# Performance work log

Measured on AMD Instinct MI355X. Metric: run time of the kernel, lower is better.

## Reference

```python
import jax, jax.numpy as jnp
import numpy as np

K = 3  # kernel_size
P = 1  # padding


def setup_inputs() -> dict:
    key = jax.random.key(0)
    k1, k2, k3 = jax.random.split(key, 3)
    B, Cin, H, W = 4, 64, 64, 64
    Cout = 64
    L = K * K + 1  # patch length + constant-1 term = 10
    x = jax.random.normal(k1, (B, Cin, H, W), dtype=jnp.float32)
    # kaiming_uniform-like scale for filters / biases
    filters = jax.random.normal(k2, (Cout, Cin, L, L), dtype=jnp.float32) * 0.05
    biases = jax.random.normal(k3, (Cout, 1), dtype=jnp.float32) * 0.05
    return {"x": x, "filters": filters, "biases": biases}


def reference(x, filters, biases):
    # x: [B, Cin, H, W]; filters: [Cout, Cin, L, L]; biases: [Cout, 1]
    B, C, H, W = x.shape
    xp = jnp.pad(x, ((0, 0), (0, 0), (P, P), (P, P)))
    # im2col: flattened KxK patch per pixel, row-major over (dy, dx) -> [B, C, K*K, H, W]
    patches = jnp.stack(
        [xp[:, :, dy:dy + H, dx:dx + W] for dy in range(K) for dx in range(K)],
        axis=2,
    )
    # prepend constant 1 -> s: [B, C, L, H, W], L = K*K + 1
    ones = jnp.ones((B, C, 1, H, W), dtype=x.dtype)
    s = jnp.concatenate([ones, patches], axis=2)
    # per-pixel, per-channel outer product s s^T: [B, C, L, L, H, W]
    outer = s[:, :, :, None, :, :] * s[:, :, None, :, :, :]
    # quadratic-form contraction with filters, summed over (c, i, j)
    out = jnp.einsum('bcijhw,ocij->bohw', outer, filters)
    out = out + biases[:, 0][None, :, None, None]
    return out
```

## Files before the change

kernel.cpp:

```cpp
#include <hip/hip_runtime.h>
#include <hip/hip_bf16.h>


typedef __attribute__((ext_vector_type(8))) short short8;
typedef __attribute__((ext_vector_type(16))) float f32x16;

#define NCH  64
#define NOUT 64

__device__ constexpr signed char TI[56] = {
  0,0,0,0,0,0,0,0,0,
  1,2,3,4,5,6,7,8,9,
  1,1,1,1,1,1,1,1,
  2,2,2,2,2,2,2,
  3,3,3,3,3,3,
  4,4,4,4,4,
  5,5,5,5,
  6,6,6,
  7,7,
  8,
  0,0};
__device__ constexpr signed char TJ[56] = {
  1,2,3,4,5,6,7,8,9,
  1,2,3,4,5,6,7,8,9,
  2,3,4,5,6,7,8,9,
  3,4,5,6,7,8,9,
  4,5,6,7,8,9,
  5,6,7,8,9,
  6,7,8,9,
  7,8,9,
  8,9,
  9,
  0,0};

__device__ __forceinline__ unsigned short f2bf(float f) {
  __hip_bfloat16 h = __float2bfloat16(f);
  unsigned short u;
  __builtin_memcpy(&u, &h, 2);
  return u;
}

__global__ __launch_bounds__(256) void prep_w2(const float* __restrict__ F,
                                               const float* __restrict__ biases,
                                               unsigned short* __restrict__ W2) {
  int idx = blockIdx.x * 256 + threadIdx.x;
  int e = idx & 7, o = (idx >> 3) & 63;
  int rest = idx >> 9;
  int hf = rest & 1, stp = rest >> 1;
  int st = stp % 7, pair = stp / 7;
  int ch = (st < 4) ? (2 * pair + hf) : (2 * pair + 1 - hf);
  int kl = (st < 4) ? (16 * st + e) : (16 * (st - 4) + 8 + e);
  const float* base = F + (size_t)(o * NCH + ch) * 100;
  float w;
  if (kl < 54) {
    int i = TI[kl], j = TJ[kl];
    if (i == 0)      w = base[j] + base[j * 10];
    else if (i == j) w = base[i * 10 + j];
    else             w = base[i * 10 + j] + base[j * 10 + i];
  } else if (kl == 54) {
    w = base[0] + (ch == 0 ? biases[o] : 0.f);
  } else {
    w = 0.f;
  }
  W2[idx] = f2bf(w);
}

__global__ __launch_bounds__(512, 2) void poly2d_mfma(
    const float* __restrict__ x, const unsigned short* __restrict__ W2,
    float* __restrict__ out) {
  const int b = blockIdx.x >> 6, h = blockIdx.x & 63;
  const int tid = threadIdx.x;
  const int lane = tid & 63, wave = tid >> 6;
  const int px = lane & 31, hf = lane >> 5;

  __shared__ float xs[NCH][3][66];
  __shared__ float R[8][64][32];

  #pragma unroll
  for (int it = 0; it < 25; ++it) {
    int idx = tid + it * 512;
    if (idx < NCH * 198) {
      int c = idx / 198, rem = idx % 198;
      int r = rem / 66, col = rem % 66;
      int hh = h + r - 1, ww = col - 1;
      float v = 0.f;
      if ((unsigned)hh < 64u && (unsigned)ww < 64u)
        v = x[(((size_t)b * NCH + c) * 64 + hh) * 64 + ww];
      xs[c][r][col] = v;
    }
  }
  __syncthreads();

  f32x16 a00, a01, a10, a11;
  #pragma unroll
  for (int r = 0; r < 16; ++r) { a00[r] = 0.f; a01[r] = 0.f; a10[r] = 0.f; a11[r] = 0.f; }

  auto computeP = [&](int cAl, int cBl, int pcol, short8* P) {
    float sA[9], sB[9];
    #pragma unroll
    for (int jm = 0; jm < 9; ++jm) {
      sA[jm] = xs[cAl][jm / 3][pcol + jm % 3];
      sB[jm] = xs[cBl][jm / 3][pcol + jm % 3];
    }
    #pragma unroll
    for (int g = 0; g < 7; ++g) {
      short8 pk;
      #pragma unroll
      for (int e = 0; e < 8; ++e) {
        const int kl = (g < 4) ? (16 * g + e) : (16 * (g - 4) + 8 + e);
        const float* s = (g < 4) ? sA : sB;
        float v;
        if (kl == 55)      v = 0.f;
        else if (kl == 54) v = 1.f;
        else if (kl < 9)   v = s[kl];
        else if (kl < 18)  { float t = s[kl - 9]; v = t * t; }
        else               v = s[TI[kl] - 1] * s[TJ[kl] - 1];
        pk[e] = (short)f2bf(v);
      }
      P[g] = pk;
    }
  };

  for (int stage = 0; stage < 4; ++stage) {
    const int cA = wave * 8 + stage * 2 + hf;
    const int cB = cA ^ 1;
    short8 P0[7], P1[7];
    computeP(cA, cB, px, P0);
    computeP(cA, cB, px + 32, P1);
    const unsigned short* wb =
        W2 + (size_t)(wave * 4 + stage) * 7168 + hf * 512 + px * 8;
    #pragma unroll
    for (int st = 0; st < 7; ++st) {
      const short8 w0 = *(const short8*)(wb + st * 1024);
      const short8 w1 = *(const short8*)(wb + st * 1024 + 256);
      a00 = __builtin_amdgcn_mfma_f32_32x32x16_bf16(w0, P0[st], a00, 0, 0, 0);
      a10 = __builtin_amdgcn_mfma_f32_32x32x16_bf16(w1, P0[st], a10, 0, 0, 0);
      a01 = __builtin_amdgcn_mfma_f32_32x32x16_bf16(w0, P1[st], a01, 0, 0, 0);
      a11 = __builtin_amdgcn_mfma_f32_32x32x16_bf16(w1, P1[st], a11, 0, 0, 0);
    }
  }

  #pragma unroll
  for (int r = 0; r < 16; ++r) {
    int orow = (r & 3) + 8 * (r >> 2) + 4 * hf;
    R[wave][orow][px]      = a00[r];
    R[wave][orow + 32][px] = a10[r];
  }
  __syncthreads();
  {
    int o = tid >> 3, p4 = (tid & 7) * 4;
    float4 sum = make_float4(0.f, 0.f, 0.f, 0.f);
    #pragma unroll
    for (int g = 0; g < 8; ++g) {
      float4 v = *(float4*)&R[g][o][p4];
      sum.x += v.x; sum.y += v.y; sum.z += v.z; sum.w += v.w;
    }
    *(float4*)&out[(((size_t)b * NOUT + o) * 64 + h) * 64 + p4] = sum;
  }
  __syncthreads();
  #pragma unroll
  for (int r = 0; r < 16; ++r) {
    int orow = (r & 3) + 8 * (r >> 2) + 4 * hf;
    R[wave][orow][px]      = a01[r];
    R[wave][orow + 32][px] = a11[r];
  }
  __syncthreads();
  {
    int o = tid >> 3, p4 = (tid & 7) * 4;
    float4 sum = make_float4(0.f, 0.f, 0.f, 0.f);
    #pragma unroll
    for (int g = 0; g < 8; ++g) {
      float4 v = *(float4*)&R[g][o][p4];
      sum.x += v.x; sum.y += v.y; sum.z += v.z; sum.w += v.w;
    }
    *(float4*)&out[(((size_t)b * NOUT + o) * 64 + h) * 64 + 32 + p4] = sum;
  }
}

extern "C" void kernel_launch(void* const* d_in, const int* in_sizes, int n_in,
                              void* d_out, int out_size, void* d_ws, size_t ws_size,
                              hipStream_t stream) {
  const float* x       = (const float*)d_in[0];
  const float* filters = (const float*)d_in[1];
  const float* biases  = (const float*)d_in[2];
  float* out = (float*)d_out;
  unsigned short* W2 = (unsigned short*)d_ws;

  hipLaunchKernelGGL(prep_w2, dim3(896), dim3(256), 0, stream,
                     filters, biases, W2);
  hipLaunchKernelGGL(poly2d_mfma, dim3(256), dim3(512), 0, stream,
                     x, W2, out);
}
```

Before: 24.25 us.

## Load per-wave channel slabs with float4, drop sync, single-pass transposed reduction

Each wave now loads only its own 8 input channels into a padded 72-wide shared slab using float4 global loads, so the block-wide barrier after staging can be removed. The patch build computes both pixel halves in one pass from shared memory. The epilogue overlays the shared buffer and writes all four accumulators at once as float4 stores into a padded transposed layout, then reduces across waves in a single pass, which removes two barriers and one reduction round. Output stores become scalar per lane, coalesced along pixels, and the larger shared footprint may lower occupancy.

```diff
diff --git a/kernel.cpp b/kernel.cpp
--- a/kernel.cpp
+++ b/kernel.cpp
@@ -73,60 +73,70 @@
   const int lane = tid & 63, wave = tid >> 6;
   const int px = lane & 31, hf = lane >> 5;
 
-  __shared__ float xs[NCH][3][66];
-  __shared__ float R[8][64][32];
+  __shared__ float smem[34816];
 
-  #pragma unroll
-  for (int it = 0; it < 25; ++it) {
-    int idx = tid + it * 512;
-    if (idx < NCH * 198) {
-      int c = idx / 198, rem = idx % 198;
-      int r = rem / 66, col = rem % 66;
-      int hh = h + r - 1, ww = col - 1;
-      float v = 0.f;
-      if ((unsigned)hh < 64u && (unsigned)ww < 64u)
-        v = x[(((size_t)b * NCH + c) * 64 + hh) * 64 + ww];
-      xs[c][r][col] = v;
+  {
+    const int r = lane >> 4, q = lane & 15;
+    const size_t xbase = ((size_t)b * NCH + wave * 8) * 4096;
+    #pragma unroll
+    for (int i = 0; i < 8; ++i) {
+      float* ch0 = &smem[(wave * 8 + i) * 216];
+      if (lane < 48) {
+        int hh = h + r - 1;
+        bool ok = (unsigned)hh < 64u;
+        int hcl = ok ? hh : 0;
+        float4 v = *(const float4*)&x[xbase + (size_t)i * 4096 + hcl * 64 + (q << 2)];
+        if (!ok) v = make_float4(0.f, 0.f, 0.f, 0.f);
+        *(float4*)&ch0[r * 72 + 4 + (q << 2)] = v;
+      } else if (lane < 54) {
+        int rr = (lane - 48) >> 1, side = lane & 1;
+        *(float4*)&ch0[rr * 72 + (side ? 68 : 0)] = make_float4(0.f, 0.f, 0.f, 0.f);
+      }
     }
   }
-  __syncthreads();
 
   f32x16 a00, a01, a10, a11;
   #pragma unroll
   for (int r = 0; r < 16; ++r) { a00[r] = 0.f; a01[r] = 0.f; a10[r] = 0.f; a11[r] = 0.f; }
 
-  auto computeP = [&](int cAl, int cBl, int pcol, short8* P) {
-    float sA[9], sB[9];
+  for (int stage = 0; stage < 4; ++stage) {
+    const int cA = stage * 2 + hf;
+    const int cB = cA ^ 1;
+    const float* rA = &smem[(wave * 8 + cA) * 216 + px];
+    const float* rB = &smem[(wave * 8 + cB) * 216 + px];
+    float sA0[9], sA1[9], sB0[9], sB1[9];
     #pragma unroll
-    for (int jm = 0; jm < 9; ++jm) {
-      sA[jm] = xs[cAl][jm / 3][pcol + jm % 3];
-      sB[jm] = xs[cBl][jm / 3][pcol + jm % 3];
+    for (int r = 0; r < 3; ++r) {
+      #pragma unroll
+      for (int d = 0; d < 3; ++d) {
+        sA0[r * 3 + d] = rA[r * 72 + 3 + d];
+        sA1[r * 3 + d] = rA[r * 72 + 35 + d];
+        sB0[r * 3 + d] = rB[r * 72 + 3 + d];
+        sB1[r * 3 + d] = rB[r * 72 + 35 + d];
+      }
     }
+    short8 P0[7], P1[7];
     #pragma unroll
     for (int g = 0; g < 7; ++g) {
-      short8 pk;
+      short8 p0, p1;
       #pragma unroll
       for (int e = 0; e < 8; ++e) {
         const int kl = (g < 4) ? (16 * g + e) : (16 * (g - 4) + 8 + e);
-        const float* s = (g < 4) ? sA : sB;
-        float v;
-        if (kl == 55)      v = 0.f;
-        else if (kl == 54) v = 1.f;
-        else if (kl < 9)   v = s[kl];
-        else if (kl < 18)  { float t = s[kl - 9]; v = t * t; }
-        else               v = s[TI[kl] - 1] * s[TJ[kl] - 1];
-        pk[e] = (short)f2bf(v);
+        const float* s0 = (g < 4) ? sA0 : sB0;
+        const float* s1 = (g < 4) ? sA1 : sB1;
+        float v0, v1;
+        if (kl == 55)      { v0 = 0.f;   v1 = 0.f; }
+        else if (kl == 54) { v0 = 1.f;   v1 = 1.f; }
+        else if (kl < 9)   { v0 = s0[kl];           v1 = s1[kl]; }
+        else if (kl < 18)  { float t0 = s0[kl - 9], t1 = s1[kl - 9];
+                             v0 = t0 * t0;          v1 = t1 * t1; }
+        else               { v0 = s0[TI[kl] - 1] * s0[TJ[kl] - 1];
+                             v1 = s1[TI[kl] - 1] * s1[TJ[kl] - 1]; }
+        p0[e] = (short)f2bf(v0);
+        p1[e] = (short)f2bf(v1);
       }
-      P[g] = pk;
+      P0[g] = p0; P1[g] = p1;
     }
-  };
-
-  for (int stage = 0; stage < 4; ++stage) {
-    const int cA = wave * 8 + stage * 2 + hf;
-    const int cB = cA ^ 1;
-    short8 P0[7], P1[7];
-    computeP(cA, cB, px, P0);
-    computeP(cA, cB, px + 32, P1);
     const unsigned short* wb =
         W2 + (size_t)(wave * 4 + stage) * 7168 + hf * 512 + px * 8;
     #pragma unroll
@@ -140,40 +150,35 @@
     }
   }
 
-  #pragma unroll
-  for (int r = 0; r < 16; ++r) {
-    int orow = (r & 3) + 8 * (r >> 2) + 4 * hf;
-    R[wave][orow][px]      = a00[r];
-    R[wave][orow + 32][px] = a10[r];
+  __syncthreads();
+  {
+    float* base0 = &smem[(wave * 64 + px) * 68];
+    float* base1 = &smem[(wave * 64 + px + 32) * 68];
+    #pragma unroll
+    for (int blk = 0; blk < 4; ++blk) {
+      int ob = blk * 8 + 4 * hf;
+      *(float4*)&base0[ob]      = make_float4(a00[blk*4], a00[blk*4+1], a00[blk*4+2], a00[blk*4+3]);
+      *(float4*)&base0[ob + 32] = make_float4(a10[blk*4], a10[blk*4+1], a10[blk*4+2], a10[blk*4+3]);
+      *(float4*)&base1[ob]      = make_float4(a01[blk*4], a01[blk*4+1], a01[blk*4+2], a01[blk*4+3]);
+      *(float4*)&base1[ob + 32] = make_float4(a11[blk*4], a11[blk*4+1], a11[blk*4+2], a11[blk*4+3]);
+    }
   }
   __syncthreads();
   {
-    int o = tid >> 3, p4 = (tid & 7) * 4;
-    float4 sum = make_float4(0.f, 0.f, 0.f, 0.f);
+    const int op = wave * 8;
+    float s8[8] = {0.f, 0.f, 0.f, 0.f, 0.f, 0.f, 0.f, 0.f};
     #pragma unroll
     for (int g = 0; g < 8; ++g) {
-      float4 v = *(float4*)&R[g][o][p4];
-      sum.x += v.x; sum.y += v.y; sum.z += v.z; sum.w += v.w;
+      const float* rg = &smem[(g * 64 + lane) * 68 + op];
+      float4 u0 = *(const float4*)&rg[0];
+      float4 u1 = *(const float4*)&rg[4];
+      s8[0] += u0.x; s8[1] += u0.y; s8[2] += u0.z; s8[3] += u0.w;
+      s8[4] += u1.x; s8[5] += u1.y; s8[6] += u1.z; s8[7] += u1.w;
     }
-    *(float4*)&out[(((size_t)b * NOUT + o) * 64 + h) * 64 + p4] = sum;
-  }
-  __syncthreads();
-  #pragma unroll
-  for (int r = 0; r < 16; ++r) {
-    int orow = (r & 3) + 8 * (r >> 2) + 4 * hf;
-    R[wave][orow][px]      = a01[r];
-    R[wave][orow + 32][px] = a11[r];
-  }
-  __syncthreads();
-  {
-    int o = tid >> 3, p4 = (tid & 7) * 4;
-    float4 sum = make_float4(0.f, 0.f, 0.f, 0.f);
+    const size_t obase = (((size_t)b * NOUT + op) * 64 + h) * 64 + lane;
     #pragma unroll
-    for (int g = 0; g < 8; ++g) {
-      float4 v = *(float4*)&R[g][o][p4];
-      sum.x += v.x; sum.y += v.y; sum.z += v.z; sum.w += v.w;
-    }
-    *(float4*)&out[(((size_t)b * NOUT + o) * 64 + h) * 64 + 32 + p4] = sum;
+    for (int k = 0; k < 8; ++k)
+      out[obase + (size_t)k * 4096] = s8[k];
   }
 }
 
```

Result: faster. 21.63 us (-10.8%).
